# Performance work log

Measured on AMD Instinct MI355X. Metric: run time of the kernel, lower is better.

Reference implementation:

```python
import jax, jax.numpy as jnp
import numpy as np

B, S, D_MODEL, HEAD = 4, 4096, 1024, 64


def rope(x):
    # Faithful to the torch code: 'odd' = even-indexed elems, 'even' = odd-indexed.
    b, s, d = x.shape
    half = d // 2
    pos = jnp.arange(s, dtype=x.dtype)
    theta = 1.0 / (10000.0 ** (jnp.arange(half, dtype=x.dtype) / half))
    freqs = pos[:, None] * theta[None, :]  # (s, half)
    sin, cos = jnp.sin(freqs), jnp.cos(freqs)
    odd = x[..., 0::2]
    even = x[..., 1::2]
    x_rot_even = even * cos + odd * sin
    x_rot_odd = odd * cos - even * sin
    return jnp.stack([x_rot_odd, x_rot_even], axis=-1).reshape(x.shape)


def setup_inputs() -> dict:
    key = jax.random.key(0)
    kx, kq, kk, kv = jax.random.split(key, 4)
    x = jax.random.normal(kx, (B, S, D_MODEL), dtype=jnp.float32)
    # torch Linear weights are [out,in]; we store the transposed [in,out] form.
    sc = 1.0 / np.sqrt(D_MODEL)
    Wq = jax.random.normal(kq, (D_MODEL, HEAD), dtype=jnp.float32) * sc
    Wk = jax.random.normal(kk, (D_MODEL, HEAD), dtype=jnp.float32) * sc
    Wv = jax.random.normal(kv, (D_MODEL, HEAD), dtype=jnp.float32) * sc
    return {"x": x, "Wq": Wq, "Wk": Wk, "Wv": Wv}


def reference(x, Wq, Wk, Wv):
    Q = rope(x @ Wq)  # (B, S, H)
    K = rope(x @ Wk)
    V = x @ Wv
    scale = K.shape[-1] ** -0.5
    scores = jnp.einsum('bqh,bkh->bqk', Q, K) * scale  # (B, S, S)
    causal = jnp.tril(jnp.ones((S, S), dtype=bool))
    scores = jnp.where(causal, scores, -jnp.inf)
    probs = jax.nn.softmax(scores, axis=-1)  # dropout p treated as 0 (eval)
    return jnp.einsum('bqk,bkh->bqh', probs, V)
```

## Files before the change

kernel.cpp:

```cpp
#include <hip/hip_runtime.h>
#include <stdint.h>


static constexpr int S_LEN  = 4096;
static constexpr int DMODEL = 1024;
static constexpr int NS     = 6;
static constexpr float SHIFT = 8.0f;

typedef __attribute__((ext_vector_type(8))) short bf16x8;
typedef __attribute__((ext_vector_type(4))) float f32x4;

#define MFMA16(a, b, c) __builtin_amdgcn_mfma_f32_16x16x32_bf16((a), (b), (c), 0, 0, 0)

__device__ __forceinline__ unsigned short f2b(float f) {
    union { float f; unsigned int u; } v;
    v.f = f;
    unsigned int u = v.u;
    u += 0x7fffu + ((u >> 16) & 1u);
    return (unsigned short)(u >> 16);
}
__device__ __forceinline__ float b2f(unsigned short b) {
    union { unsigned int u; float f; } v;
    v.u = ((unsigned int)b) << 16;
    return v.f;
}

template <int CTRL>
__device__ __forceinline__ float dpp_f(float v) {
    return __builtin_bit_cast(float,
        __builtin_amdgcn_update_dpp(0, __builtin_bit_cast(int, v), CTRL, 0xf, 0xf, false));
}
__device__ __forceinline__ float rowsum16(float v) {
    v += dpp_f<0x128>(v);
    v += dpp_f<0x124>(v);
    v += dpp_f<0x122>(v);
    v += dpp_f<0x121>(v);
    return v;
}

__device__ __forceinline__ void dma16(const void* g, void* l) {
    __builtin_amdgcn_global_load_lds(
        (const __attribute__((address_space(1))) unsigned int*)g,
        (__attribute__((address_space(3))) unsigned int*)l, 16, 0, 0);
}

__global__ __launch_bounds__(256) void prep_wt(const float* __restrict__ Wq,
                                               const float* __restrict__ Wk,
                                               const float* __restrict__ Wv,
                                               unsigned short* __restrict__ Wt) {
    int idx = blockIdx.x * 256 + threadIdx.x;
    int c = idx >> 10;
    int k = idx & 1023;
    int mat = c >> 6, n = c & 63;
    const float* W = (mat == 0) ? Wq : (mat == 1) ? Wk : Wv;
    Wt[idx] = f2b(W[k * 64 + n]);
}

__global__ __launch_bounds__(256, 2) void proj_rope(const float* __restrict__ x,
                                                    const unsigned short* __restrict__ Wt,
                                                    unsigned short* __restrict__ Qg,
                                                    unsigned short* __restrict__ Kg,
                                                    unsigned short* __restrict__ Vtg) {
    __shared__ __align__(16) float          Xs[2][64 * 64];
    __shared__ __align__(16) unsigned short Bs[2][96 * 64];

    const int tid  = threadIdx.x;
    const int wave = tid >> 6, lane = tid & 63;
    const int l15  = lane & 15, quad = lane >> 4;
    const int rbase = (blockIdx.x >> 1) * 64;
    const int ch    = blockIdx.x & 1;

    f32x4 acc[6];
#pragma unroll
    for (int ft = 0; ft < 6; ++ft) acc[ft] = (f32x4){0.f, 0.f, 0.f, 0.f};

    const float* xg = x + (size_t)rbase * DMODEL;
    const unsigned short* wg = Wt + (size_t)(ch * 96) * 1024;

    auto stage = [&](int kc, int buf) {
#pragma unroll
        for (int ii = 0; ii < 4; ++ii) {
            const int i = 4 * wave + ii;
            const int row = i * 4 + (lane >> 4);
            const int gd = lane & 15;
            const int gs = (gd & 8) | ((gd & 7) ^ (row & 7));
            dma16(xg + (size_t)row * DMODEL + kc * 64 + gs * 4, &Xs[buf][i * 256]);
        }
#pragma unroll
        for (int jj = 0; jj < 3; ++jj) {
            const int j = 3 * wave + jj;
            const int col = j * 8 + (lane >> 3);
            const int gd = lane & 7;
            const int gs = gd ^ (col & 7);
            dma16(wg + (size_t)col * 1024 + kc * 64 + gs * 8, &Bs[buf][j * 512]);
        }
    };

    stage(0, 0);
    int p = 0;
    const int msk = l15 & 7;

#pragma unroll 1
    for (int kc = 0; kc < 16; ++kc) {
        __syncthreads();
        if (kc + 1 < 16) stage(kc + 1, p ^ 1);

        const float* Xb = &Xs[p][0];
        const unsigned short* Bb = &Bs[p][0];
        const int arow = wave * 16 + l15;

#pragma unroll
        for (int kk2 = 0; kk2 < 2; ++kk2) {
            float4 a0 = *reinterpret_cast<const float4*>(
                Xb + arow * 64 + (kk2 * 8 + ((quad * 2) ^ msk)) * 4);
            float4 a1 = *reinterpret_cast<const float4*>(
                Xb + arow * 64 + (kk2 * 8 + ((quad * 2 + 1) ^ msk)) * 4);
            bf16x8 af;
            af[0] = (short)f2b(a0.x); af[1] = (short)f2b(a0.y);
            af[2] = (short)f2b(a0.z); af[3] = (short)f2b(a0.w);
            af[4] = (short)f2b(a1.x); af[5] = (short)f2b(a1.y);
            af[6] = (short)f2b(a1.z); af[7] = (short)f2b(a1.w);
#pragma unroll
            for (int ft = 0; ft < 6; ++ft) {
                bf16x8 bf = *reinterpret_cast<const bf16x8*>(
                    Bb + (ft * 16 + l15) * 64 + ((kk2 * 4 + quad) ^ msk) * 8);
                acc[ft] = MFMA16(af, bf, acc[ft]);
            }
        }
        p ^= 1;
    }

#pragma unroll
    for (int ft = 0; ft < 6; ++ft) {
        const int col0 = ch * 96 + ft * 16;
        const int mat  = col0 >> 6;
        const int d    = (col0 & 63) + l15;
        float theta = 0.f;
        if (mat < 2) {
            int i = d >> 1;
            theta = exp2f((float)i * -0.41524101186f);
        }
#pragma unroll
        for (int r = 0; r < 4; ++r) {
            const int gr   = rbase + wave * 16 + quad * 4 + r;
            const int b    = gr >> 12;
            const int spos = gr & (S_LEN - 1);
            float v = acc[ft][r];
            if (mat < 2) {
                float partner = __shfl_xor(v, 1);
                float fr = (float)spos * theta;
                float sn = __sinf(fr);
                float cs = __cosf(fr);
                float outv = (d & 1) ? (v * cs + partner * sn)
                                     : (v * cs - partner * sn);
                if (mat == 0) outv *= 0.125f;
                unsigned short bv = f2b(outv);
                if (mat == 0) Qg[(size_t)gr * 64 + d] = bv;
                else          Kg[(size_t)gr * 64 + d] = bv;
            } else {
                Vtg[(size_t)b * (64 * S_LEN) + (size_t)d * S_LEN + spos] = f2b(v);
            }
        }
    }
}

__global__ __launch_bounds__(256) void attn_split(const unsigned short* __restrict__ Qg,
                                                  const unsigned short* __restrict__ Kg,
                                                  const unsigned short* __restrict__ Vtg,
                                                  unsigned short* __restrict__ OP,
                                                  float* __restrict__ L) {
    __shared__ __align__(16) unsigned short Klds[2][64 * 64];
    __shared__ __align__(16) unsigned short Vlds[2][64 * 64];
    __shared__ __align__(16) unsigned short Plds[4][16 * 72];

    const int tid  = threadIdx.x;
    const int wave = tid >> 6, lane = tid & 63;
    const int l15  = lane & 15, quad = lane >> 4;
    const int qt = 63 - blockIdx.x;
    const int split = blockIdx.y, b = blockIdx.z;
    const int qbase = qt * 64;

    const int total = qt + 1;
    const int chunk = (total + NS - 1) / NS;
    const int k0 = split * chunk;
    const int k1 = (k0 + chunk < total) ? (k0 + chunk) : total;

    bf16x8 qa[2];
    {
        const unsigned short* qrow = Qg + (size_t)(b * S_LEN + qbase + wave * 16 + l15) * 64;
        qa[0] = *reinterpret_cast<const bf16x8*>(qrow + quad * 8);
        qa[1] = *reinterpret_cast<const bf16x8*>(qrow + 32 + quad * 8);
    }

    f32x4 o[4];
    float lsum[4];
#pragma unroll
    for (int nt = 0; nt < 4; ++nt) o[nt] = (f32x4){0.f, 0.f, 0.f, 0.f};
#pragma unroll
    for (int r = 0; r < 4; ++r) lsum[r] = 0.f;

    const unsigned short* kgb = Kg  + (size_t)(b * S_LEN) * 64;
    const unsigned short* vgb = Vtg + (size_t)b * (64 * S_LEN);
    unsigned short* Pw = &Plds[wave][0];

    const int i0 = 2 * wave, i1 = 2 * wave + 1;
    const int r0 = (i0 * 64 + lane) >> 3, g0 = (i0 * 64 + lane) & 7;
    const int r1 = (i1 * 64 + lane) >> 3, g1 = (i1 * 64 + lane) & 7;
    const int sg0 = (g0 ^ (r0 & 7)) * 8, sg1 = (g1 ^ (r1 & 7)) * 8;

    auto stage = [&](int kt, int buf) {
        const unsigned short* kp = kgb + (size_t)kt * 64 * 64;
        dma16(kp + r0 * 64 + sg0, &Klds[buf][i0 * 512]);
        dma16(kp + r1 * 64 + sg1, &Klds[buf][i1 * 512]);
        const unsigned short* vp = vgb + (size_t)kt * 64;
        dma16(vp + (size_t)r0 * S_LEN + sg0, &Vlds[buf][i0 * 512]);
        dma16(vp + (size_t)r1 * S_LEN + sg1, &Vlds[buf][i1 * 512]);
    };

    if (k0 < k1) stage(k0, 0);

    int p = 0;
    for (int kt = k0; kt < k1; ++kt) {
        __syncthreads();
        if (kt + 1 < k1) stage(kt + 1, p ^ 1);

        const unsigned short* Kb = &Klds[p][0];
        const unsigned short* Vb = &Vlds[p][0];

        f32x4 s[4];
#pragma unroll
        for (int nt = 0; nt < 4; ++nt) {
            const int rk = nt * 16 + l15;
            bf16x8 kb0 = *reinterpret_cast<const bf16x8*>(Kb + rk * 64 + ((quad ^ (rk & 7)) * 8));
            bf16x8 kb1 = *reinterpret_cast<const bf16x8*>(Kb + rk * 64 + (((4 + quad) ^ (rk & 7)) * 8));
            f32x4 z = (f32x4){0.f, 0.f, 0.f, 0.f};
            z = MFMA16(qa[0], kb0, z);
            z = MFMA16(qa[1], kb1, z);
            s[nt] = z;
        }

        if (kt == qt) {
#pragma unroll
            for (int nt = 0; nt < 4; ++nt) {
                int key_l = nt * 16 + l15;
#pragma unroll
                for (int r = 0; r < 4; ++r) {
                    int q_l = wave * 16 + quad * 4 + r;
                    if (key_l > q_l) s[nt][r] = -1e30f;
                }
            }
        }

#pragma unroll
        for (int nt = 0; nt < 4; ++nt)
#pragma unroll
            for (int r = 0; r < 4; ++r) {
                float pv = __expf(s[nt][r] - SHIFT);
                s[nt][r] = pv;
                lsum[r] += pv;
            }

#pragma unroll
        for (int nt = 0; nt < 4; ++nt)
#pragma unroll
            for (int r = 0; r < 4; ++r)
                Pw[(quad * 4 + r) * 72 + nt * 16 + l15] = f2b(s[nt][r]);

#pragma unroll
        for (int kc = 0; kc < 2; ++kc) {
            bf16x8 pa = *reinterpret_cast<const bf16x8*>(Pw + l15 * 72 + kc * 32 + quad * 8);
#pragma unroll
            for (int nt = 0; nt < 4; ++nt) {
                const int rv = nt * 16 + l15;
                bf16x8 vb = *reinterpret_cast<const bf16x8*>(
                    Vb + rv * 64 + (((kc * 4 + quad) ^ (rv & 7)) * 8));
                o[nt] = MFMA16(pa, vb, o[nt]);
            }
        }
        p ^= 1;
    }

#pragma unroll
    for (int r = 0; r < 4; ++r) lsum[r] = rowsum16(lsum[r]);

    const size_t prow_base = ((size_t)(split * 4 + b)) * S_LEN;
#pragma unroll
    for (int nt = 0; nt < 4; ++nt)
#pragma unroll
        for (int r = 0; r < 4; ++r) {
            int row = qbase + wave * 16 + quad * 4 + r;
            OP[(prow_base + row) * 64 + nt * 16 + l15] = f2b(o[nt][r]);
        }
    if (l15 == 0) {
#pragma unroll
        for (int r = 0; r < 4; ++r) {
            int row = qbase + wave * 16 + quad * 4 + r;
            L[prow_base + row] = lsum[r];
        }
    }
}

__global__ __launch_bounds__(256) void combine(const unsigned short* __restrict__ OP,
                                               const float* __restrict__ L,
                                               float* __restrict__ out) {
    int idx = blockIdx.x * 256 + threadIdx.x;
    int d   = idx & 63;
    int row = (idx >> 6) & (S_LEN - 1);
    int b   = idx >> 18;

    float num = 0.f, den = 0.f;
#pragma unroll
    for (int s = 0; s < NS; ++s) {
        size_t pr = (size_t)(s * 4 + b) * S_LEN + row;
        den += L[pr];
        num += b2f(OP[pr * 64 + d]);
    }
    out[idx] = num / den;
}

extern "C" void kernel_launch(void* const* d_in, const int* in_sizes, int n_in,
                              void* d_out, int out_size, void* d_ws, size_t ws_size,
                              hipStream_t stream) {
    const float* x  = (const float*)d_in[0];
    const float* Wq = (const float*)d_in[1];
    const float* Wk = (const float*)d_in[2];
    const float* Wv = (const float*)d_in[3];
    float* out = (float*)d_out;

    unsigned char* base = (unsigned char*)d_ws;
    unsigned short* Qg  = (unsigned short*)(base);
    unsigned short* Kg  = (unsigned short*)(base + (2u << 20));
    unsigned short* Vtg = (unsigned short*)(base + (4u << 20));
    unsigned short* Wt  = (unsigned short*)(base + (6u << 20));
    float*          L   = (float*)(base + (6u << 20) + (1u << 19));
    unsigned short* OP  = (unsigned short*)(base + (7u << 20));

    prep_wt<<<768, 256, 0, stream>>>(Wq, Wk, Wv, Wt);
    proj_rope<<<512, 256, 0, stream>>>(x, Wt, Qg, Kg, Vtg);
    attn_split<<<dim3(64, NS, 4), 256, 0, stream>>>(Qg, Kg, Vtg, OP, L);
    combine<<<4096, 256, 0, stream>>>(OP, L, out);
}
```

Before: 156.5 us.

## Double query tile per block to reuse K/V tiles across two row fragments

Each attention block now handles 128 query rows (two 64-row fragments per wave pair) instead of 64, so every staged K/V tile in LDS feeds twice as many MFMAs. The split count rises from 6 to 8 to keep the grid populated after halving the query-tile count. The causal mask now applies to the last two key tiles using global indices. The cost is higher register pressure from doubled accumulators, more partial outputs for the combine kernel to read, and more work wasted on masked keys in the diagonal tiles.

```diff
diff --git a/kernel.cpp b/kernel.cpp
--- a/kernel.cpp
+++ b/kernel.cpp
@@ -4,7 +4,7 @@
 
 static constexpr int S_LEN  = 4096;
 static constexpr int DMODEL = 1024;
-static constexpr int NS     = 6;
+static constexpr int NS     = 8;
 static constexpr float SHIFT = 8.0f;
 
 typedef __attribute__((ext_vector_type(8))) short bf16x8;
@@ -171,33 +171,38 @@
                                                   float* __restrict__ L) {
     __shared__ __align__(16) unsigned short Klds[2][64 * 64];
     __shared__ __align__(16) unsigned short Vlds[2][64 * 64];
-    __shared__ __align__(16) unsigned short Plds[4][16 * 72];
+    __shared__ __align__(16) unsigned short Plds[4][32 * 72];
 
     const int tid  = threadIdx.x;
     const int wave = tid >> 6, lane = tid & 63;
     const int l15  = lane & 15, quad = lane >> 4;
-    const int qt = 63 - blockIdx.x;
+    const int qt = 31 - blockIdx.x;
     const int split = blockIdx.y, b = blockIdx.z;
-    const int qbase = qt * 64;
-
-    const int total = qt + 1;
+    const int qbase = qt * 128;
+
+    const int total = 2 * qt + 2;
     const int chunk = (total + NS - 1) / NS;
     const int k0 = split * chunk;
     const int k1 = (k0 + chunk < total) ? (k0 + chunk) : total;
 
-    bf16x8 qa[2];
-    {
-        const unsigned short* qrow = Qg + (size_t)(b * S_LEN + qbase + wave * 16 + l15) * 64;
-        qa[0] = *reinterpret_cast<const bf16x8*>(qrow + quad * 8);
-        qa[1] = *reinterpret_cast<const bf16x8*>(qrow + 32 + quad * 8);
-    }
-
-    f32x4 o[4];
-    float lsum[4];
-#pragma unroll
-    for (int nt = 0; nt < 4; ++nt) o[nt] = (f32x4){0.f, 0.f, 0.f, 0.f};
-#pragma unroll
-    for (int r = 0; r < 4; ++r) lsum[r] = 0.f;
+    bf16x8 qa[2][2];
+#pragma unroll
+    for (int mf = 0; mf < 2; ++mf) {
+        const unsigned short* qrow =
+            Qg + (size_t)(b * S_LEN + qbase + mf * 64 + wave * 16 + l15) * 64;
+        qa[mf][0] = *reinterpret_cast<const bf16x8*>(qrow + quad * 8);
+        qa[mf][1] = *reinterpret_cast<const bf16x8*>(qrow + 32 + quad * 8);
+    }
+
+    f32x4 o[2][4];
+    float lsum[2][4];
+#pragma unroll
+    for (int mf = 0; mf < 2; ++mf)
+#pragma unroll
+        for (int nt = 0; nt < 4; ++nt) {
+            o[mf][nt] = (f32x4){0.f, 0.f, 0.f, 0.f};
+            lsum[mf][nt] = 0.f;
+        }
 
     const unsigned short* kgb = Kg  + (size_t)(b * S_LEN) * 64;
     const unsigned short* vgb = Vtg + (size_t)b * (64 * S_LEN);
@@ -227,75 +232,92 @@
         const unsigned short* Kb = &Klds[p][0];
         const unsigned short* Vb = &Vlds[p][0];
 
-        f32x4 s[4];
+        f32x4 s[2][4];
 #pragma unroll
         for (int nt = 0; nt < 4; ++nt) {
             const int rk = nt * 16 + l15;
             bf16x8 kb0 = *reinterpret_cast<const bf16x8*>(Kb + rk * 64 + ((quad ^ (rk & 7)) * 8));
             bf16x8 kb1 = *reinterpret_cast<const bf16x8*>(Kb + rk * 64 + (((4 + quad) ^ (rk & 7)) * 8));
-            f32x4 z = (f32x4){0.f, 0.f, 0.f, 0.f};
-            z = MFMA16(qa[0], kb0, z);
-            z = MFMA16(qa[1], kb1, z);
-            s[nt] = z;
-        }
-
-        if (kt == qt) {
-#pragma unroll
-            for (int nt = 0; nt < 4; ++nt) {
-                int key_l = nt * 16 + l15;
+#pragma unroll
+            for (int mf = 0; mf < 2; ++mf) {
+                f32x4 z = (f32x4){0.f, 0.f, 0.f, 0.f};
+                z = MFMA16(qa[mf][0], kb0, z);
+                z = MFMA16(qa[mf][1], kb1, z);
+                s[mf][nt] = z;
+            }
+        }
+
+        if (kt >= 2 * qt) {
+            const int kb0g = kt * 64;
+#pragma unroll
+            for (int mf = 0; mf < 2; ++mf)
+#pragma unroll
+                for (int nt = 0; nt < 4; ++nt) {
+                    int key_g = kb0g + nt * 16 + l15;
+#pragma unroll
+                    for (int r = 0; r < 4; ++r) {
+                        int q_g = qbase + mf * 64 + wave * 16 + quad * 4 + r;
+                        if (key_g > q_g) s[mf][nt][r] = -1e30f;
+                    }
+                }
+        }
+
+#pragma unroll
+        for (int mf = 0; mf < 2; ++mf)
+#pragma unroll
+            for (int nt = 0; nt < 4; ++nt)
 #pragma unroll
                 for (int r = 0; r < 4; ++r) {
-                    int q_l = wave * 16 + quad * 4 + r;
-                    if (key_l > q_l) s[nt][r] = -1e30f;
+                    float pv = __expf(s[mf][nt][r] - SHIFT);
+                    s[mf][nt][r] = pv;
+                    lsum[mf][r] += pv;
                 }
-            }
-        }
-
-#pragma unroll
-        for (int nt = 0; nt < 4; ++nt)
-#pragma unroll
-            for (int r = 0; r < 4; ++r) {
-                float pv = __expf(s[nt][r] - SHIFT);
-                s[nt][r] = pv;
-                lsum[r] += pv;
-            }
-
-#pragma unroll
-        for (int nt = 0; nt < 4; ++nt)
-#pragma unroll
-            for (int r = 0; r < 4; ++r)
-                Pw[(quad * 4 + r) * 72 + nt * 16 + l15] = f2b(s[nt][r]);
+
+#pragma unroll
+        for (int mf = 0; mf < 2; ++mf)
+#pragma unroll
+            for (int nt = 0; nt < 4; ++nt)
+#pragma unroll
+                for (int r = 0; r < 4; ++r)
+                    Pw[(mf * 16 + quad * 4 + r) * 72 + nt * 16 + l15] = f2b(s[mf][nt][r]);
 
 #pragma unroll
         for (int kc = 0; kc < 2; ++kc) {
-            bf16x8 pa = *reinterpret_cast<const bf16x8*>(Pw + l15 * 72 + kc * 32 + quad * 8);
+            bf16x8 pa0 = *reinterpret_cast<const bf16x8*>(Pw + (0 * 16 + l15) * 72 + kc * 32 + quad * 8);
+            bf16x8 pa1 = *reinterpret_cast<const bf16x8*>(Pw + (1 * 16 + l15) * 72 + kc * 32 + quad * 8);
 #pragma unroll
             for (int nt = 0; nt < 4; ++nt) {
                 const int rv = nt * 16 + l15;
                 bf16x8 vb = *reinterpret_cast<const bf16x8*>(
                     Vb + rv * 64 + (((kc * 4 + quad) ^ (rv & 7)) * 8));
-                o[nt] = MFMA16(pa, vb, o[nt]);
+                o[0][nt] = MFMA16(pa0, vb, o[0][nt]);
+                o[1][nt] = MFMA16(pa1, vb, o[1][nt]);
             }
         }
         p ^= 1;
     }
 
 #pragma unroll
-    for (int r = 0; r < 4; ++r) lsum[r] = rowsum16(lsum[r]);
+    for (int mf = 0; mf < 2; ++mf)
+#pragma unroll
+        for (int r = 0; r < 4; ++r) lsum[mf][r] = rowsum16(lsum[mf][r]);
 
     const size_t prow_base = ((size_t)(split * 4 + b)) * S_LEN;
 #pragma unroll
-    for (int nt = 0; nt < 4; ++nt)
-#pragma unroll
-        for (int r = 0; r < 4; ++r) {
-            int row = qbase + wave * 16 + quad * 4 + r;
-            OP[(prow_base + row) * 64 + nt * 16 + l15] = f2b(o[nt][r]);
-        }
-    if (l15 == 0) {
-#pragma unroll
-        for (int r = 0; r < 4; ++r) {
-            int row = qbase + wave * 16 + quad * 4 + r;
-            L[prow_base + row] = lsum[r];
+    for (int mf = 0; mf < 2; ++mf) {
+#pragma unroll
+        for (int nt = 0; nt < 4; ++nt)
+#pragma unroll
+            for (int r = 0; r < 4; ++r) {
+                int row = qbase + mf * 64 + wave * 16 + quad * 4 + r;
+                OP[(prow_base + row) * 64 + nt * 16 + l15] = f2b(o[mf][nt][r]);
+            }
+        if (l15 == 0) {
+#pragma unroll
+            for (int r = 0; r < 4; ++r) {
+                int row = qbase + mf * 64 + wave * 16 + quad * 4 + r;
+                L[prow_base + row] = lsum[mf][r];
+            }
         }
     }
 }
@@ -337,6 +359,6 @@
 
     prep_wt<<<768, 256, 0, stream>>>(Wq, Wk, Wv, Wt);
     proj_rope<<<512, 256, 0, stream>>>(x, Wt, Qg, Kg, Vtg);
-    attn_split<<<dim3(64, NS, 4), 256, 0, stream>>>(Qg, Kg, Vtg, OP, L);
+    attn_split<<<dim3(32, NS, 4), 256, 0, stream>>>(Qg, Kg, Vtg, OP, L);
     combine<<<4096, 256, 0, stream>>>(OP, L, out);
 }
```

Result: slower. 161.6 us (+3.3%).

## Compute transposed scores so P feeds PV MFMA from registers without LDS

Applied to the files above, without the earlier changes.

The QK^T product is swapped to K·Q^T so each lane holds four key scores for one query row, which are packed directly into an fp16 operand for a 16x16x16 f16 MFMA against V. The per-wave P staging buffer in LDS, its stores and reloads are removed. V is now stored as fp16 instead of bf16 to match the f16 MFMA. The row-sum reduction becomes cross-quad shuffles, and output stores become packed 4-element writes. This uses twice as many smaller MFMAs for PV in exchange for eliminating the LDS round trip.

```diff
diff --git a/kernel.cpp b/kernel.cpp
--- a/kernel.cpp
+++ b/kernel.cpp
@@ -9,8 +9,11 @@
 
 typedef __attribute__((ext_vector_type(8))) short bf16x8;
 typedef __attribute__((ext_vector_type(4))) float f32x4;
-
-#define MFMA16(a, b, c) __builtin_amdgcn_mfma_f32_16x16x32_bf16((a), (b), (c), 0, 0, 0)
+typedef __attribute__((ext_vector_type(4))) _Float16 f16x4;
+typedef __attribute__((ext_vector_type(4))) unsigned short u16x4;
+
+#define MFMA16(a, b, c)  __builtin_amdgcn_mfma_f32_16x16x32_bf16((a), (b), (c), 0, 0, 0)
+#define MFMAH16(a, b, c) __builtin_amdgcn_mfma_f32_16x16x16f16((a), (b), (c), 0, 0, 0)
 
 __device__ __forceinline__ unsigned short f2b(float f) {
     union { float f; unsigned int u; } v;
@@ -24,18 +27,9 @@
     v.u = ((unsigned int)b) << 16;
     return v.f;
 }
-
-template <int CTRL>
-__device__ __forceinline__ float dpp_f(float v) {
-    return __builtin_bit_cast(float,
-        __builtin_amdgcn_update_dpp(0, __builtin_bit_cast(int, v), CTRL, 0xf, 0xf, false));
-}
-__device__ __forceinline__ float rowsum16(float v) {
-    v += dpp_f<0x128>(v);
-    v += dpp_f<0x124>(v);
-    v += dpp_f<0x122>(v);
-    v += dpp_f<0x121>(v);
-    return v;
+__device__ __forceinline__ unsigned short f2h(float f) {
+    _Float16 h = (_Float16)f;
+    return __builtin_bit_cast(unsigned short, h);
 }
 
 __device__ __forceinline__ void dma16(const void* g, void* l) {
@@ -158,7 +152,7 @@
                 if (mat == 0) Qg[(size_t)gr * 64 + d] = bv;
                 else          Kg[(size_t)gr * 64 + d] = bv;
             } else {
-                Vtg[(size_t)b * (64 * S_LEN) + (size_t)d * S_LEN + spos] = f2b(v);
+                Vtg[(size_t)b * (64 * S_LEN) + (size_t)d * S_LEN + spos] = f2h(v);
             }
         }
     }
@@ -171,7 +165,6 @@
                                                   float* __restrict__ L) {
     __shared__ __align__(16) unsigned short Klds[2][64 * 64];
     __shared__ __align__(16) unsigned short Vlds[2][64 * 64];
-    __shared__ __align__(16) unsigned short Plds[4][16 * 72];
 
     const int tid  = threadIdx.x;
     const int wave = tid >> 6, lane = tid & 63;
@@ -185,23 +178,20 @@
     const int k0 = split * chunk;
     const int k1 = (k0 + chunk < total) ? (k0 + chunk) : total;
 
-    bf16x8 qa[2];
+    bf16x8 qb[2];
     {
         const unsigned short* qrow = Qg + (size_t)(b * S_LEN + qbase + wave * 16 + l15) * 64;
-        qa[0] = *reinterpret_cast<const bf16x8*>(qrow + quad * 8);
-        qa[1] = *reinterpret_cast<const bf16x8*>(qrow + 32 + quad * 8);
+        qb[0] = *reinterpret_cast<const bf16x8*>(qrow + quad * 8);
+        qb[1] = *reinterpret_cast<const bf16x8*>(qrow + 32 + quad * 8);
     }
 
     f32x4 o[4];
-    float lsum[4];
-#pragma unroll
-    for (int nt = 0; nt < 4; ++nt) o[nt] = (f32x4){0.f, 0.f, 0.f, 0.f};
-#pragma unroll
-    for (int r = 0; r < 4; ++r) lsum[r] = 0.f;
+    float lsum = 0.f;
+#pragma unroll
+    for (int dt = 0; dt < 4; ++dt) o[dt] = (f32x4){0.f, 0.f, 0.f, 0.f};
 
     const unsigned short* kgb = Kg  + (size_t)(b * S_LEN) * 64;
     const unsigned short* vgb = Vtg + (size_t)b * (64 * S_LEN);
-    unsigned short* Pw = &Plds[wave][0];
 
     const int i0 = 2 * wave, i1 = 2 * wave + 1;
     const int r0 = (i0 * 64 + lane) >> 3, g0 = (i0 * 64 + lane) & 7;
@@ -227,77 +217,55 @@
         const unsigned short* Kb = &Klds[p][0];
         const unsigned short* Vb = &Vlds[p][0];
 
-        f32x4 s[4];
-#pragma unroll
-        for (int nt = 0; nt < 4; ++nt) {
-            const int rk = nt * 16 + l15;
-            bf16x8 kb0 = *reinterpret_cast<const bf16x8*>(Kb + rk * 64 + ((quad ^ (rk & 7)) * 8));
-            bf16x8 kb1 = *reinterpret_cast<const bf16x8*>(Kb + rk * 64 + (((4 + quad) ^ (rk & 7)) * 8));
+#pragma unroll
+        for (int sub = 0; sub < 4; ++sub) {
+            const int rk = sub * 16 + l15;
+            bf16x8 ka0 = *reinterpret_cast<const bf16x8*>(Kb + rk * 64 + ((quad ^ (rk & 7)) * 8));
+            bf16x8 ka1 = *reinterpret_cast<const bf16x8*>(Kb + rk * 64 + (((4 + quad) ^ (rk & 7)) * 8));
             f32x4 z = (f32x4){0.f, 0.f, 0.f, 0.f};
-            z = MFMA16(qa[0], kb0, z);
-            z = MFMA16(qa[1], kb1, z);
-            s[nt] = z;
-        }
-
-        if (kt == qt) {
-#pragma unroll
-            for (int nt = 0; nt < 4; ++nt) {
-                int key_l = nt * 16 + l15;
+            z = MFMA16(ka0, qb[0], z);
+            z = MFMA16(ka1, qb[1], z);
+
+            if (kt == qt) {
+                const int qg = wave * 16 + l15;
 #pragma unroll
                 for (int r = 0; r < 4; ++r) {
-                    int q_l = wave * 16 + quad * 4 + r;
-                    if (key_l > q_l) s[nt][r] = -1e30f;
+                    int key_l = sub * 16 + quad * 4 + r;
+                    if (key_l > qg) z[r] = -1e30f;
                 }
             }
-        }
-
-#pragma unroll
-        for (int nt = 0; nt < 4; ++nt)
+
+            f16x4 pf;
 #pragma unroll
             for (int r = 0; r < 4; ++r) {
-                float pv = __expf(s[nt][r] - SHIFT);
-                s[nt][r] = pv;
-                lsum[r] += pv;
-            }
-
-#pragma unroll
-        for (int nt = 0; nt < 4; ++nt)
-#pragma unroll
-            for (int r = 0; r < 4; ++r)
-                Pw[(quad * 4 + r) * 72 + nt * 16 + l15] = f2b(s[nt][r]);
-
-#pragma unroll
-        for (int kc = 0; kc < 2; ++kc) {
-            bf16x8 pa = *reinterpret_cast<const bf16x8*>(Pw + l15 * 72 + kc * 32 + quad * 8);
-#pragma unroll
-            for (int nt = 0; nt < 4; ++nt) {
-                const int rv = nt * 16 + l15;
-                bf16x8 vb = *reinterpret_cast<const bf16x8*>(
-                    Vb + rv * 64 + (((kc * 4 + quad) ^ (rv & 7)) * 8));
-                o[nt] = MFMA16(pa, vb, o[nt]);
+                float pv = __expf(z[r] - SHIFT);
+                lsum += pv;
+                pf[r] = (_Float16)pv;
+            }
+
+#pragma unroll
+            for (int dt = 0; dt < 4; ++dt) {
+                const int rv = dt * 16 + l15;
+                f16x4 va = *reinterpret_cast<const f16x4*>(
+                    Vb + rv * 64 + (((sub * 2 + (quad >> 1)) ^ (rv & 7)) * 8) + (quad & 1) * 4);
+                o[dt] = MFMAH16(va, pf, o[dt]);
             }
         }
         p ^= 1;
     }
 
-#pragma unroll
-    for (int r = 0; r < 4; ++r) lsum[r] = rowsum16(lsum[r]);
-
-    const size_t prow_base = ((size_t)(split * 4 + b)) * S_LEN;
-#pragma unroll
-    for (int nt = 0; nt < 4; ++nt)
-#pragma unroll
-        for (int r = 0; r < 4; ++r) {
-            int row = qbase + wave * 16 + quad * 4 + r;
-            OP[(prow_base + row) * 64 + nt * 16 + l15] = f2b(o[nt][r]);
-        }
-    if (l15 == 0) {
-#pragma unroll
-        for (int r = 0; r < 4; ++r) {
-            int row = qbase + wave * 16 + quad * 4 + r;
-            L[prow_base + row] = lsum[r];
-        }
-    }
+    lsum += __shfl_xor(lsum, 16);
+    lsum += __shfl_xor(lsum, 32);
+
+    const size_t prow = ((size_t)(split * 4 + b)) * S_LEN + qbase + wave * 16 + l15;
+#pragma unroll
+    for (int dt = 0; dt < 4; ++dt) {
+        u16x4 pk;
+#pragma unroll
+        for (int r = 0; r < 4; ++r) pk[r] = f2b(o[dt][r]);
+        *reinterpret_cast<u16x4*>(OP + prow * 64 + dt * 16 + quad * 4) = pk;
+    }
+    if (quad == 0) L[prow] = lsum;
 }
 
 __global__ __launch_bounds__(256) void combine(const unsigned short* __restrict__ OP,
```

Result: no change. 158.2 us (+1.0%).
